# Kernel tuning notes

Hardware: AMD Instinct MI355X
Metric: run time of the kernel (lower is better)

## Reference

```python
import jax, jax.numpy as jnp
import numpy as np
import math

H = 4096; NH = 32; QLR = 1536; KVLR = 512
DN = 128; DR = 64; DV = 128; QD = DN + DR  # q_head_dim = 192
B = 1; S = 2048
BASE = 50000.0; FACTOR = 32.0; ORIG_MAX = 4096; BETA_FAST = 32.0; BETA_SLOW = 1.0
EPS = 1e-6
_M = 0.1 * 1.0 * math.log(FACTOR) + 1.0  # yarn mscale (mscale_all_dim=1)
SCALE = (QD ** -0.5) * _M * _M


def _yarn_cos_sin(seq_len):
    dim = DR
    f = np.arange(0, dim, 2, dtype=np.float32) / dim
    freq_extra = 1.0 / BASE ** f
    freq_inter = 1.0 / (FACTOR * BASE ** f)
    def corr(nr):
        return dim * math.log(ORIG_MAX / (nr * 2 * math.pi)) / (2 * math.log(BASE))
    low = max(math.floor(corr(BETA_FAST)), 0)
    high = min(math.ceil(corr(BETA_SLOW)), dim - 1)
    hi = high + 0.001 if low == high else float(high)
    ramp = np.clip((np.arange(dim // 2, dtype=np.float32) - low) / (hi - low), 0.0, 1.0)
    inv_freq_mask = 1.0 - ramp
    inv_freq = freq_inter * (1.0 - inv_freq_mask) + freq_extra * inv_freq_mask
    t = np.arange(seq_len, dtype=np.float32)
    fr = np.outer(t, inv_freq)
    emb = np.concatenate([fr, fr], axis=-1)
    # mscale ratio = get_mscale(f,1)/get_mscale(f,1) = 1.0
    return jnp.asarray(np.cos(emb)), jnp.asarray(np.sin(emb))


def _rms(x, w):
    v = jnp.mean(x.astype(jnp.float32) ** 2, axis=-1, keepdims=True)
    return w * (x.astype(jnp.float32) * jax.lax.rsqrt(v + EPS)).astype(x.dtype)


def _reorder(x):
    # interleaved -> [evens, odds] (matches view(d//2,2).transpose.reshape)
    d = x.shape[-1]
    x = x.reshape(x.shape[:-1] + (d // 2, 2))
    return jnp.concatenate([x[..., 0], x[..., 1]], axis=-1)


def _rotate_half(x):
    h = x.shape[-1] // 2
    return jnp.concatenate([-x[..., h:], x[..., :h]], axis=-1)


def _rope(x, cos, sin):
    x = _reorder(x)
    return x * cos + _rotate_half(x) * sin


def setup_inputs() -> dict:
    key = jax.random.key(0)
    ks = jax.random.split(key, 6)
    hs = jax.random.normal(ks[0], (B, S, H), dtype=jnp.float32)
    causal = jnp.tril(jnp.ones((S, S), dtype=bool))
    mask = jnp.where(causal, 0.0, -1e9).astype(jnp.float32)[None, None]
    pos = jnp.broadcast_to(jnp.arange(S, dtype=jnp.int64 if jax.config.jax_enable_x64 else jnp.int32), (B, S))
    def w(k, shape, fan_in):
        return jax.random.normal(k, shape, dtype=jnp.float32) * (fan_in ** -0.5)
    return {
        "hidden_states": hs,
        "attention_mask": mask,
        "position_ids": pos,
        "q_a_w": w(ks[1], (QLR, H), H),
        "q_a_ln_w": jnp.ones((QLR,), jnp.float32),
        "q_b_w": w(ks[2], (NH * QD, QLR), QLR),
        "kv_a_w": w(ks[3], (KVLR + DR, H), H),
        "kv_a_ln_w": jnp.ones((KVLR,), jnp.float32),
        "kv_b_w": w(ks[4], (NH * (DN + DV), KVLR), KVLR),
        "o_w": w(ks[5], (H, NH * DV), NH * DV),
    }


def reference(hidden_states, attention_mask, position_ids, q_a_w, q_a_ln_w, q_b_w, kv_a_w, kv_a_ln_w, kv_b_w, o_w):
    b, s, _ = hidden_states.shape
    q = _rms(hidden_states @ q_a_w.T, q_a_ln_w) @ q_b_w.T
    q = q.reshape(b, s, NH, QD).transpose(0, 2, 1, 3)          # [b,h,s,192]
    q_nope, q_pe = q[..., :DN], q[..., DN:]
    ckv = hidden_states @ kv_a_w.T                              # [b,s,576]
    comp, k_pe = ckv[..., :KVLR], ckv[..., KVLR:]
    k_pe = k_pe.reshape(b, s, 1, DR).transpose(0, 2, 1, 3)      # [b,1,s,64]
    kv = (_rms(comp, kv_a_ln_w) @ kv_b_w.T).reshape(b, s, NH, DN + DV).transpose(0, 2, 1, 3)
    k_nope, v = kv[..., :DN], kv[..., DN:]
    cos, sin = _yarn_cos_sin(s)
    cos = cos[position_ids][:, None]                            # [b,1,s,64]
    sin = sin[position_ids][:, None]
    q_pe = _rope(q_pe, cos, sin)
    k_pe = _rope(k_pe, cos, sin)
    qs = jnp.concatenate([q_nope, q_pe], axis=-1)               # [b,h,s,192]
    ks = jnp.concatenate([k_nope, jnp.broadcast_to(k_pe, (b, NH, s, DR))], axis=-1)
    aw = jnp.einsum('bhqd,bhkd->bhqk', qs, ks) * SCALE
    aw = jax.nn.softmax((aw + attention_mask).astype(jnp.float32), axis=-1).astype(hidden_states.dtype)
    out = jnp.einsum('bhqk,bhkd->bhqd', aw, v)                  # [b,h,s,128]
    out = out.transpose(0, 2, 1, 3).reshape(b, s, NH * DV)
    return out @ o_w.T
```

## Files before the change

### kernel.cpp

```cpp
#include <hip/hip_runtime.h>
#include <hip/hip_fp16.h>

typedef _Float16 f16x8 __attribute__((ext_vector_type(8)));
typedef float f32x4 __attribute__((ext_vector_type(4)));

#define DEV __device__ __forceinline__

typedef const __attribute__((address_space(1))) void gvoid_t;
typedef __attribute__((address_space(3))) void lvoid_t;

DEV void gload16(const void* g, void* l) {
  __builtin_amdgcn_global_load_lds((gvoid_t*)g, (lvoid_t*)l, 16, 0, 0);
}

DEV f32x4 mfma16(f16x8 a, f16x8 b, f32x4 c) {
  return __builtin_amdgcn_mfma_f32_16x16x32_f16(a, b, c, 0, 0, 0);
}

__global__ __launch_bounds__(256) void cvt_kernel(const float* __restrict__ s,
                                                  __half* __restrict__ d, int n4) {
  int stride = gridDim.x * 256;
  for (int i = blockIdx.x * 256 + threadIdx.x; i < n4; i += stride) {
    float4 v = ((const float4*)s)[i];
    __align__(8) __half a[4] = {__float2half(v.x), __float2half(v.y),
                                __float2half(v.z), __float2half(v.w)};
    *((uint2*)(d + (size_t)i * 4)) = *((uint2*)a);
  }
}

template <int W>
__global__ __launch_bounds__(256) void rms_kernel(const float* __restrict__ x, int ldx,
                                                  const float* __restrict__ wgt,
                                                  __half* __restrict__ y, int ldy) {
  const int row = blockIdx.x, tid = threadIdx.x;
  const float4* xr = (const float4*)(x + (size_t)row * ldx);
  float4 v0 = make_float4(0.f, 0.f, 0.f, 0.f), v1 = v0;
  if (tid < W / 4) v0 = xr[tid];
  if (tid + 256 < W / 4) v1 = xr[tid + 256];
  float ss = v0.x * v0.x + v0.y * v0.y + v0.z * v0.z + v0.w * v0.w +
             v1.x * v1.x + v1.y * v1.y + v1.z * v1.z + v1.w * v1.w;
  for (int mm = 1; mm <= 32; mm <<= 1) ss += __shfl_xor(ss, mm);
  __shared__ float sred[4];
  if ((tid & 63) == 0) sred[tid >> 6] = ss;
  __syncthreads();
  float rs = 1.0f / sqrtf((sred[0] + sred[1] + sred[2] + sred[3]) * (1.0f / (float)W) + 1e-6f);
  __half* yr = y + (size_t)row * ldy;
  if (tid < W / 4) {
    int j = tid * 4;
    yr[j + 0] = __float2half(wgt[j + 0] * v0.x * rs);
    yr[j + 1] = __float2half(wgt[j + 1] * v0.y * rs);
    yr[j + 2] = __float2half(wgt[j + 2] * v0.z * rs);
    yr[j + 3] = __float2half(wgt[j + 3] * v0.w * rs);
  }
  if (tid + 256 < W / 4) {
    int j = (tid + 256) * 4;
    yr[j + 0] = __float2half(wgt[j + 0] * v1.x * rs);
    yr[j + 1] = __float2half(wgt[j + 1] * v1.y * rs);
    yr[j + 2] = __float2half(wgt[j + 2] * v1.z * rs);
    yr[j + 3] = __float2half(wgt[j + 3] * v1.w * rs);
  }
}

__global__ __launch_bounds__(256) void rope_table_kernel(const int* __restrict__ pos,
                                                         float2* __restrict__ cs) {
  int i = blockIdx.x * 256 + threadIdx.x;
  int row = i >> 5, j = i & 31;
  double f = (double)j * (1.0 / 32.0);
  double fe = exp(-f * 10.81977828441028);
  double fi = fe * (1.0 / 32.0);
  double ramp = fmin(fmax(((double)j - 8.0) * (1.0 / 12.0), 0.0), 1.0);
  double inv = fi * ramp + fe * (1.0 - ramp);
  double ang = (double)pos[row] * inv;
  cs[i] = make_float2((float)cos(ang), (float)sin(ang));
}

__global__ __launch_bounds__(256) void rope_q_kernel(const __half* __restrict__ qpe,
                                                     const float2* __restrict__ cs,
                                                     __half* __restrict__ Qb, float qscale) {
  int i = blockIdx.x * 256 + threadIdx.x;
  int row = i >> 10, rem = i & 1023, h = rem >> 5, j = rem & 31;
  float x0 = __half2float(qpe[(size_t)row * 2048 + h * 64 + 2 * j]);
  float x1 = __half2float(qpe[(size_t)row * 2048 + h * 64 + 2 * j + 1]);
  float2 c = cs[row * 32 + j];
  float o0 = (x0 * c.x - x1 * c.y) * qscale;
  float o1 = (x1 * c.x + x0 * c.y) * qscale;
  __half* dst = Qb + ((size_t)h * 2048 + row) * 192;
  dst[128 + j] = __float2half(o0);
  dst[160 + j] = __float2half(o1);
}

__global__ __launch_bounds__(256) void rope_k_kernel(const float* __restrict__ kpe, int ld,
                                                     const float2* __restrict__ cs,
                                                     __half* __restrict__ Kb) {
  int i = blockIdx.x * 256 + threadIdx.x;
  int row = i >> 10, rem = i & 1023, h = rem >> 5, j = rem & 31;
  float x0 = kpe[(size_t)row * ld + 2 * j];
  float x1 = kpe[(size_t)row * ld + 2 * j + 1];
  float2 c = cs[row * 32 + j];
  __half* dst = Kb + ((size_t)h * 2048 + row) * 192;
  dst[128 + j] = __float2half(x0 * c.x - x1 * c.y);
  dst[160 + j] = __float2half(x1 * c.x + x0 * c.y);
}

template <int EPI>
__global__ __launch_bounds__(256) void gemm128(const __half* __restrict__ A, int lda,
                                               const __half* __restrict__ B, int K, int Ncols,
                                               float* __restrict__ Cf, int ldc,
                                               __half* __restrict__ O1, __half* __restrict__ O2,
                                               float qscale) {
  __shared__ __align__(16) char As[8192];
  __shared__ __align__(16) char Bs[8192];
  const int tid = threadIdx.x;
  const int lane = tid & 63, w = tid >> 6;
  const int l15 = lane & 15, g = lane >> 4;
  const int wr = w >> 1, wc = w & 1;
  const int nwg = gridDim.x * gridDim.y;
  int wg = blockIdx.y * gridDim.x + blockIdx.x;
  wg = (wg & 7) * (nwg >> 3) + (wg >> 3);
  const int m0 = (wg / gridDim.x) * 128, n0 = (wg % gridDim.x) * 128;
  const int srow = lane >> 2, scol = (lane & 3) * 8;
  f32x4 acc[4][4] = {};

  for (int kt = 0; kt < K; kt += 32) {
    __syncthreads();
#pragma unroll
    for (int cc = 0; cc < 2; ++cc) {
      int c = 2 * w + cc;
      gload16(A + (size_t)(m0 + c * 16 + srow) * lda + kt + scol, As + c * 1024);
      gload16(B + (size_t)(n0 + c * 16 + srow) * K + kt + scol, Bs + c * 1024);
    }
    __syncthreads();
    f16x8 af[4], bf[4];
#pragma unroll
    for (int m = 0; m < 4; ++m)
      af[m] = *(const f16x8*)(As + (wr * 64 + m * 16 + l15) * 64 + g * 16);
#pragma unroll
    for (int n = 0; n < 4; ++n)
      bf[n] = *(const f16x8*)(Bs + (wc * 64 + n * 16 + l15) * 64 + g * 16);
#pragma unroll
    for (int m = 0; m < 4; ++m)
#pragma unroll
      for (int n = 0; n < 4; ++n) acc[m][n] = mfma16(af[m], bf[n], acc[m][n]);
  }

#pragma unroll
  for (int m = 0; m < 4; ++m)
#pragma unroll
    for (int n = 0; n < 4; ++n)
#pragma unroll
      for (int i = 0; i < 4; ++i) {
        int row = m0 + wr * 64 + m * 16 + g * 4 + i;
        int col = n0 + wc * 64 + n * 16 + l15;
        float v = acc[m][n][i];
        if (EPI == 0) {
          if (col < Ncols) Cf[(size_t)row * ldc + col] = v;
        } else if (EPI == 2) {
          int h = col / 192, d = col - h * 192;
          if (d < 128)
            O1[((size_t)h * 2048 + row) * 192 + d] = __float2half(v * qscale);
          else
            O2[(size_t)row * 2048 + h * 64 + (d - 128)] = __float2half(v);
        } else if (EPI == 3) {
          int h = col >> 8, d = col & 255;
          if (d < 128)
            O1[((size_t)h * 2048 + row) * 192 + d] = __float2half(v);
          else
            O2[((size_t)h * 128 + (d - 128)) * 2048 + row] = __float2half(v);
        }
      }
}

__global__ __launch_bounds__(256) void attn_kernel(const __half* __restrict__ Q,
                                                   const __half* __restrict__ K,
                                                   const __half* __restrict__ Vt,
                                                   __half* __restrict__ Out) {
  __shared__ __align__(16) char Klds[2 * 64 * 384];
  __shared__ __align__(16) char Vlds[128 * 128];
  __shared__ __align__(16) __half Plds[4][16][72];
  int wg = blockIdx.y * gridDim.x + blockIdx.x;
  wg = (wg & 7) * 64 + (wg >> 3);
  const int pr = wg & 15, h = wg >> 4;
  const int tid = threadIdx.x, lane = tid & 63, w = tid >> 6;
  const int l15 = lane & 15, g = lane >> 4;

  const char* Kg = (const char*)(K + (size_t)h * 2048 * 192);
  const char* Vg = (const char*)(Vt + (size_t)h * 128 * 2048);

  int kL[6], kRow[6], kSS[6];
#pragma unroll
  for (int cc = 0; cc < 6; ++cc) {
    int c = w * 6 + cc;
    int L = c * 64 + lane;
    int row = (L * 2731) >> 16;
    int slot = L - row * 24;
    kL[cc] = c;
    kRow[cc] = row;
    kSS[cc] = (slot & ~7) | ((slot ^ row) & 7);
  }

  for (int ht = 0; ht < 2; ++ht) {
    const int qt = ht ? (31 - pr) : pr;
    const int q0 = qt * 64;
    const int nt = qt + 1;

    const __half* Qh = Q + ((size_t)h * 2048 + q0 + w * 16 + l15) * 192;
    f16x8 qf[6];
#pragma unroll
    for (int kc = 0; kc < 6; ++kc) qf[kc] = *(const f16x8*)(Qh + kc * 32 + g * 8);

    f32x4 acc[8] = {};
    float m_i[4], l_i[4];
#pragma unroll
    for (int i = 0; i < 4; ++i) { m_i[i] = -1e30f; l_i[i] = 0.f; }

#pragma unroll
    for (int cc = 0; cc < 6; ++cc)
      gload16(Kg + (size_t)kRow[cc] * 384 + kSS[cc] * 16, Klds + kL[cc] * 1024);
    __syncthreads();

    for (int t = 0; t < nt; ++t) {
      const int kv0 = t * 64;
      const char* Kcur = Klds + (t & 1) * 24576;

#pragma unroll
      for (int cc = 0; cc < 4; ++cc) {
        int c = w * 4 + cc;
        int L = c * 64 + lane;
        int d = L >> 3, slot = L & 7;
        int ss = slot ^ (d & 7);
        gload16(Vg + ((size_t)d * 2048 + kv0) * 2 + ss * 16, Vlds + c * 1024);
      }
      if (t + 1 < nt) {
        char* Knxt = Klds + ((t + 1) & 1) * 24576;
#pragma unroll
        for (int cc = 0; cc < 6; ++cc)
          gload16(Kg + (size_t)(kv0 + 64 + kRow[cc]) * 384 + kSS[cc] * 16,
                  Knxt + kL[cc] * 1024);
      }

      f32x4 s[4] = {};
#pragma unroll
      for (int kc = 0; kc < 6; ++kc) {
#pragma unroll
        for (int n = 0; n < 4; ++n) {
          int krow = n * 16 + l15;
          int slot = kc * 4 + g;
          int ss = (slot & ~7) | ((slot ^ krow) & 7);
          f16x8 kf = *(const f16x8*)(Kcur + krow * 384 + ss * 16);
          s[n] = mfma16(qf[kc], kf, s[n]);
        }
      }

      const bool diag = (t == nt - 1);
      float ps[4][4];
      float mt[4] = {-1e30f, -1e30f, -1e30f, -1e30f};
#pragma unroll
      for (int n = 0; n < 4; ++n)
#pragma unroll
        for (int i = 0; i < 4; ++i) {
          float v = s[n][i];
          if (diag) {
            int key = n * 16 + l15, qq = w * 16 + g * 4 + i;
            if (key > qq) v = -1e30f;
          }
          ps[n][i] = v;
          mt[i] = fmaxf(mt[i], v);
        }
#pragma unroll
      for (int mm = 1; mm <= 8; mm <<= 1)
#pragma unroll
        for (int i = 0; i < 4; ++i) mt[i] = fmaxf(mt[i], __shfl_xor(mt[i], mm));
      float corr[4], rsum[4];
#pragma unroll
      for (int i = 0; i < 4; ++i) {
        float mn = fmaxf(m_i[i], mt[i]);
        corr[i] = __expf(m_i[i] - mn);
        m_i[i] = mn;
        rsum[i] = 0.f;
      }
#pragma unroll
      for (int n = 0; n < 4; ++n)
#pragma unroll
        for (int i = 0; i < 4; ++i) {
          float p = __expf(ps[n][i] - m_i[i]);
          ps[n][i] = p;
          rsum[i] += p;
        }
#pragma unroll
      for (int mm = 1; mm <= 8; mm <<= 1)
#pragma unroll
        for (int i = 0; i < 4; ++i) rsum[i] += __shfl_xor(rsum[i], mm);
#pragma unroll
      for (int i = 0; i < 4; ++i) l_i[i] = l_i[i] * corr[i] + rsum[i];
#pragma unroll
      for (int db = 0; db < 8; ++db)
#pragma unroll
        for (int i = 0; i < 4; ++i) acc[db][i] *= corr[i];
#pragma unroll
      for (int n = 0; n < 4; ++n)
#pragma unroll
        for (int i = 0; i < 4; ++i) Plds[w][g * 4 + i][n * 16 + l15] = __float2half(ps[n][i]);

      __syncthreads();

#pragma unroll
      for (int ks = 0; ks < 2; ++ks) {
        f16x8 pa = *(const f16x8*)((const char*)&Plds[w][0][0] + l15 * 144 + ks * 64 + g * 16);
#pragma unroll
        for (int db = 0; db < 8; ++db) {
          int d = db * 16 + l15;
          int ss = (ks * 4 + g) ^ (d & 7);
          f16x8 vf = *(const f16x8*)(Vlds + d * 128 + ss * 16);
          acc[db] = mfma16(pa, vf, acc[db]);
        }
      }
      __syncthreads();
    }

#pragma unroll
    for (int db = 0; db < 8; ++db)
#pragma unroll
      for (int i = 0; i < 4; ++i) {
        int row = q0 + w * 16 + g * 4 + i;
        Out[(size_t)row * 4096 + h * 128 + db * 16 + l15] = __float2half(acc[db][i] / l_i[i]);
      }
  }
}

extern "C" void kernel_launch(void* const* d_in, const int* in_sizes, int n_in,
                              void* d_out, int out_size, void* d_ws, size_t ws_size,
                              hipStream_t stream) {
  (void)in_sizes; (void)n_in; (void)out_size; (void)ws_size;
  const float* hs = (const float*)d_in[0];
  const int* pos = (const int*)d_in[2];
  const float* q_a_w = (const float*)d_in[3];
  const float* q_a_ln = (const float*)d_in[4];
  const float* q_b_w = (const float*)d_in[5];
  const float* kv_a_w = (const float*)d_in[6];
  const float* kv_a_ln = (const float*)d_in[7];
  const float* kv_b_w = (const float*)d_in[8];
  const float* o_w = (const float*)d_in[9];

  char* p = (char*)d_ws;
  auto alloc = [&](size_t sz) { char* r = p; p += (sz + 255) & ~(size_t)255; return r; };
  __half* hs_h = (__half*)alloc((size_t)2048 * 4096 * 2);
  __half* w_qab = (__half*)alloc((size_t)2176 * 4096 * 2);
  __half* w_qb = (__half*)alloc((size_t)6144 * 1536 * 2);
  __half* w_kvb = (__half*)alloc((size_t)8192 * 512 * 2);
  float* qab_f = (float*)alloc((size_t)2048 * 2112 * 4);
  __half* qa_r = (__half*)alloc((size_t)2048 * 1536 * 2);
  __half* kv_r = (__half*)alloc((size_t)2048 * 512 * 2);
  float2* cs_tab = (float2*)alloc((size_t)2048 * 32 * 8);
  __half* Qb = (__half*)alloc((size_t)32 * 2048 * 192 * 2);
  __half* Kb = (__half*)alloc((size_t)32 * 2048 * 192 * 2);
  __half* Vtb = (__half*)alloc((size_t)32 * 128 * 2048 * 2);
  __half* qpe = (__half*)alloc((size_t)2048 * 2048 * 2);
  __half* attn_h = hs_h;
  __half* w_o = Qb;

  constexpr float QSCALE = 0.13086090981960297f;

  auto cvt = [&](const float* s, __half* d, size_t n) {
    int n4 = (int)(n / 4);
    int grid = (n4 + 255) / 256;
    if (grid > 2048) grid = 2048;
    cvt_kernel<<<grid, 256, 0, stream>>>(s, d, n4);
  };

  cvt(hs, hs_h, (size_t)2048 * 4096);
  cvt(q_a_w, w_qab, (size_t)1536 * 4096);
  cvt(kv_a_w, w_qab + (size_t)1536 * 4096, (size_t)576 * 4096);
  cvt(q_b_w, w_qb, (size_t)6144 * 1536);
  cvt(kv_b_w, w_kvb, (size_t)8192 * 512);
  rope_table_kernel<<<(2048 * 32) / 256, 256, 0, stream>>>(pos, cs_tab);

  gemm128<0><<<dim3(17, 16), 256, 0, stream>>>(hs_h, 4096, w_qab, 4096, 2112, qab_f, 2112,
                                               nullptr, nullptr, 1.f);
  rms_kernel<1536><<<2048, 256, 0, stream>>>(qab_f, 2112, q_a_ln, qa_r, 1536);
  rms_kernel<512><<<2048, 256, 0, stream>>>(qab_f + 1536, 2112, kv_a_ln, kv_r, 512);
  rope_k_kernel<<<(2048 * 1024) / 256, 256, 0, stream>>>(qab_f + 2048, 2112, cs_tab, Kb);
  gemm128<2><<<dim3(48, 16), 256, 0, stream>>>(qa_r, 1536, w_qb, 1536, 6144, nullptr, 0,
                                               Qb, qpe, QSCALE);
  rope_q_kernel<<<(2048 * 1024) / 256, 256, 0, stream>>>(qpe, cs_tab, Qb, QSCALE);
  gemm128<3><<<dim3(64, 16), 256, 0, stream>>>(kv_r, 512, w_kvb, 512, 8192, nullptr, 0,
                                               Kb, Vtb, 1.f);
  attn_kernel<<<dim3(16, 32), 256, 0, stream>>>(Qb, Kb, Vtb, attn_h);
  cvt(o_w, w_o, (size_t)4096 * 4096);
  gemm128<0><<<dim3(32, 16), 256, 0, stream>>>(attn_h, 4096, w_o, 4096, 4096, (float*)d_out,
                                               4096, nullptr, nullptr, 1.f);
}
```

Before: 500.3 us.

## Double-buffer GEMM with swizzled 64-wide K tiles, fuse conversions, prioritize MFMA

The GEMM moves from a single-buffered K=32 loop to a double-buffered K=64 loop. The next tile's global-to-LDS loads are issued while MFMAs run on the current tile, and an XOR swizzle is applied to avoid LDS bank conflicts. The five input fp32→fp16 conversions are merged into one launch to cut launch overhead. The attention kernel raises wave priority around its MFMA sections. LDS use per GEMM block grows from 16KB to 64KB, which may lower occupancy.

```diff
diff --git a/kernel.cpp b/kernel.cpp
--- a/kernel.cpp
+++ b/kernel.cpp
@@ -25,6 +25,32 @@
     __align__(8) __half a[4] = {__float2half(v.x), __float2half(v.y),
                                 __float2half(v.z), __float2half(v.w)};
     *((uint2*)(d + (size_t)i * 4)) = *((uint2*)a);
+  }
+}
+
+__global__ __launch_bounds__(256) void cvt5_kernel(const float* __restrict__ s0,
+                                                   const float* __restrict__ s1,
+                                                   const float* __restrict__ s2,
+                                                   const float* __restrict__ s3,
+                                                   const float* __restrict__ s4,
+                                                   __half* __restrict__ d0, __half* __restrict__ d1,
+                                                   __half* __restrict__ d2, __half* __restrict__ d3,
+                                                   __half* __restrict__ d4) {
+  const int c0 = 2097152, c1 = 3670016, c2 = 4259840, c3 = 6619136, c4 = 7667712;
+  int stride = gridDim.x * 256;
+  for (int i = blockIdx.x * 256 + threadIdx.x; i < c4; i += stride) {
+    const float* s;
+    __half* d;
+    int j;
+    if (i < c0) { s = s0; d = d0; j = i; }
+    else if (i < c1) { s = s1; d = d1; j = i - c0; }
+    else if (i < c2) { s = s2; d = d2; j = i - c1; }
+    else if (i < c3) { s = s3; d = d3; j = i - c2; }
+    else { s = s4; d = d4; j = i - c3; }
+    float4 v = ((const float4*)s)[j];
+    __align__(8) __half a[4] = {__float2half(v.x), __float2half(v.y),
+                                __float2half(v.z), __float2half(v.w)};
+    *((uint2*)(d + (size_t)j * 4)) = *((uint2*)a);
   }
 }
 
@@ -108,8 +134,8 @@
                                                float* __restrict__ Cf, int ldc,
                                                __half* __restrict__ O1, __half* __restrict__ O2,
                                                float qscale) {
-  __shared__ __align__(16) char As[8192];
-  __shared__ __align__(16) char Bs[8192];
+  __shared__ __align__(16) char As[32768];
+  __shared__ __align__(16) char Bs[32768];
   const int tid = threadIdx.x;
   const int lane = tid & 63, w = tid >> 6;
   const int l15 = lane & 15, g = lane >> 4;
@@ -118,29 +144,49 @@
   int wg = blockIdx.y * gridDim.x + blockIdx.x;
   wg = (wg & 7) * (nwg >> 3) + (wg >> 3);
   const int m0 = (wg / gridDim.x) * 128, n0 = (wg % gridDim.x) * 128;
-  const int srow = lane >> 2, scol = (lane & 3) * 8;
+  const int srow = lane >> 3;
+  const int scol = ((lane & 7) ^ srow) * 8;
   f32x4 acc[4][4] = {};
-
-  for (int kt = 0; kt < K; kt += 32) {
-    __syncthreads();
-#pragma unroll
-    for (int cc = 0; cc < 2; ++cc) {
-      int c = 2 * w + cc;
-      gload16(A + (size_t)(m0 + c * 16 + srow) * lda + kt + scol, As + c * 1024);
-      gload16(B + (size_t)(n0 + c * 16 + srow) * K + kt + scol, Bs + c * 1024);
+  const int nt = K >> 6;
+
+  auto stage = [&](int t, int buf) {
+    const __half* Ab = A + t * 64 + scol;
+    const __half* Bb = B + t * 64 + scol;
+#pragma unroll
+    for (int cc = 0; cc < 4; ++cc) {
+      int ch = w * 4 + cc;
+      gload16(Ab + (size_t)(m0 + ch * 8 + srow) * lda, As + buf * 16384 + ch * 1024);
+      gload16(Bb + (size_t)(n0 + ch * 8 + srow) * K, Bs + buf * 16384 + ch * 1024);
+    }
+  };
+
+  stage(0, 0);
+  __syncthreads();
+
+  for (int t = 0; t < nt; ++t) {
+    const int buf = t & 1;
+    if (t + 1 < nt) stage(t + 1, buf ^ 1);
+    const char* Ab = As + buf * 16384;
+    const char* Bb = Bs + buf * 16384;
+#pragma unroll
+    for (int kk = 0; kk < 2; ++kk) {
+      f16x8 af[4], bf[4];
+#pragma unroll
+      for (int m = 0; m < 4; ++m) {
+        int r = wr * 64 + m * 16 + l15;
+        af[m] = *(const f16x8*)(Ab + r * 128 + (((kk << 2) | g) ^ (r & 7)) * 16);
+      }
+#pragma unroll
+      for (int n = 0; n < 4; ++n) {
+        int r = wc * 64 + n * 16 + l15;
+        bf[n] = *(const f16x8*)(Bb + r * 128 + (((kk << 2) | g) ^ (r & 7)) * 16);
+      }
+#pragma unroll
+      for (int m = 0; m < 4; ++m)
+#pragma unroll
+        for (int n = 0; n < 4; ++n) acc[m][n] = mfma16(af[m], bf[n], acc[m][n]);
     }
     __syncthreads();
-    f16x8 af[4], bf[4];
-#pragma unroll
-    for (int m = 0; m < 4; ++m)
-      af[m] = *(const f16x8*)(As + (wr * 64 + m * 16 + l15) * 64 + g * 16);
-#pragma unroll
-    for (int n = 0; n < 4; ++n)
-      bf[n] = *(const f16x8*)(Bs + (wc * 64 + n * 16 + l15) * 64 + g * 16);
-#pragma unroll
-    for (int m = 0; m < 4; ++m)
-#pragma unroll
-      for (int n = 0; n < 4; ++n) acc[m][n] = mfma16(af[m], bf[n], acc[m][n]);
   }
 
 #pragma unroll
@@ -239,6 +285,7 @@
       }
 
       f32x4 s[4] = {};
+      __builtin_amdgcn_s_setprio(1);
 #pragma unroll
       for (int kc = 0; kc < 6; ++kc) {
 #pragma unroll
@@ -250,6 +297,7 @@
           s[n] = mfma16(qf[kc], kf, s[n]);
         }
       }
+      __builtin_amdgcn_s_setprio(0);
 
       const bool diag = (t == nt - 1);
       float ps[4][4];
@@ -303,6 +351,7 @@
 
       __syncthreads();
 
+      __builtin_amdgcn_s_setprio(1);
 #pragma unroll
       for (int ks = 0; ks < 2; ++ks) {
         f16x8 pa = *(const f16x8*)((const char*)&Plds[w][0][0] + l15 * 144 + ks * 64 + g * 16);
@@ -314,6 +363,7 @@
           acc[db] = mfma16(pa, vf, acc[db]);
         }
       }
+      __builtin_amdgcn_s_setprio(0);
       __syncthreads();
     }
 
@@ -360,18 +410,9 @@
 
   constexpr float QSCALE = 0.13086090981960297f;
 
-  auto cvt = [&](const float* s, __half* d, size_t n) {
-    int n4 = (int)(n / 4);
-    int grid = (n4 + 255) / 256;
-    if (grid > 2048) grid = 2048;
-    cvt_kernel<<<grid, 256, 0, stream>>>(s, d, n4);
-  };
-
-  cvt(hs, hs_h, (size_t)2048 * 4096);
-  cvt(q_a_w, w_qab, (size_t)1536 * 4096);
-  cvt(kv_a_w, w_qab + (size_t)1536 * 4096, (size_t)576 * 4096);
-  cvt(q_b_w, w_qb, (size_t)6144 * 1536);
-  cvt(kv_b_w, w_kvb, (size_t)8192 * 512);
+  cvt5_kernel<<<2048, 256, 0, stream>>>(hs, q_a_w, kv_a_w, q_b_w, kv_b_w,
+                                        hs_h, w_qab, w_qab + (size_t)1536 * 4096,
+                                        w_qb, w_kvb);
   rope_table_kernel<<<(2048 * 32) / 256, 256, 0, stream>>>(pos, cs_tab);
 
   gemm128<0><<<dim3(17, 16), 256, 0, stream>>>(hs_h, 4096, w_qab, 4096, 2112, qab_f, 2112,
@@ -385,7 +426,7 @@
   gemm128<3><<<dim3(64, 16), 256, 0, stream>>>(kv_r, 512, w_kvb, 512, 8192, nullptr, 0,
                                                Kb, Vtb, 1.f);
   attn_kernel<<<dim3(16, 32), 256, 0, stream>>>(Qb, Kb, Vtb, attn_h);
-  cvt(o_w, w_o, (size_t)4096 * 4096);
+  cvt_kernel<<<2048, 256, 0, stream>>>(o_w, w_o, (int)((size_t)4096 * 4096 / 4));
   gemm128<0><<<dim3(32, 16), 256, 0, stream>>>(attn_h, 4096, w_o, 4096, 4096, (float*)d_out,
                                                4096, nullptr, nullptr, 1.f);
 }
```

Measured after the change: 441.0 us. 1.13x faster.
